# Optimization experiments

Measured on AMD Instinct MI355X. Metric: run time of the kernel, lower is better.

The kernel has to match this reference:

```python
import jax, jax.numpy as jnp
import numpy as np

N, E, P = 50000, 1600000, 500000
IN_DIM, HID, OUT = 512, 128, 64
EPS = 1e-5


def setup_inputs() -> dict:
    key = jax.random.key(0)
    ks = jax.random.split(key, 16)
    d = {}
    d['x'] = jax.random.normal(ks[0], (N, IN_DIM), dtype=jnp.float32)
    d['ei'] = jax.random.randint(ks[1], (2, E), 0, N, dtype=jnp.int32)
    d['src'] = jax.random.randint(ks[2], (P,), 0, N, dtype=jnp.int32)
    d['dst'] = jax.random.randint(ks[3], (P,), 0, N, dtype=jnp.int32)
    # GCNConv layer 1 params
    d['W1'] = jax.random.normal(ks[4], (IN_DIM, HID), dtype=jnp.float32) / np.sqrt(IN_DIM)
    d['b1'] = jnp.zeros((HID,), jnp.float32)
    d['bn1_gamma'] = jnp.ones((HID,), jnp.float32)
    d['bn1_beta'] = jnp.zeros((HID,), jnp.float32)
    d['bn1_mean'] = jnp.zeros((HID,), jnp.float32)
    d['bn1_var'] = jnp.ones((HID,), jnp.float32)
    # GCNConv layer 2 params
    d['W2'] = jax.random.normal(ks[5], (HID, OUT), dtype=jnp.float32) / np.sqrt(HID)
    d['b2'] = jnp.zeros((OUT,), jnp.float32)
    d['bn2_gamma'] = jnp.ones((OUT,), jnp.float32)
    d['bn2_beta'] = jnp.zeros((OUT,), jnp.float32)
    d['bn2_mean'] = jnp.zeros((OUT,), jnp.float32)
    d['bn2_var'] = jnp.ones((OUT,), jnp.float32)
    # edge head MLP
    d['hW1'] = jax.random.normal(ks[6], (2 * OUT, OUT), dtype=jnp.float32) / np.sqrt(2 * OUT)
    d['hb1'] = jnp.zeros((OUT,), jnp.float32)
    d['hW2'] = jax.random.normal(ks[7], (OUT, 1), dtype=jnp.float32) / np.sqrt(OUT)
    d['hb2'] = jnp.zeros((1,), jnp.float32)
    return d


def gcn_conv(x, ei, W, b):
    """PyG-style GCNConv: add self-loops, symmetric deg^-1/2 normalization."""
    xw = x @ W  # [N, F]
    row, col = ei[0], ei[1]
    ones = jnp.ones((ei.shape[1],), x.dtype)
    deg = jax.ops.segment_sum(ones, col, num_segments=N) + 1.0  # +1 for self-loop
    dinv = jax.lax.rsqrt(deg)
    norm = dinv[row] * dinv[col]  # [E]
    agg = jax.ops.segment_sum(norm[:, None] * xw[row], col, num_segments=N)
    # self-loop contribution: dinv[i]^2 * xw[i]
    return agg + (dinv * dinv)[:, None] * xw + b


def bn_eval(x, gamma, beta, mean, var):
    return (x - mean) * jax.lax.rsqrt(var + EPS) * gamma + beta


def reference(x, ei, src, dst, W1, b1, bn1_gamma, bn1_beta, bn1_mean, bn1_var,
              W2, b2, bn2_gamma, bn2_beta, bn2_mean, bn2_var, hW1, hb1, hW2, hb2):
    h = jax.nn.relu(bn_eval(gcn_conv(x, ei, W1, b1), bn1_gamma, bn1_beta, bn1_mean, bn1_var))
    # dropout is identity in eval mode
    z = jax.nn.relu(bn_eval(gcn_conv(h, ei, W2, b2), bn2_gamma, bn2_beta, bn2_mean, bn2_var))
    pair = jnp.concatenate([z[src], z[dst]], axis=1)  # [P, 2*OUT]
    hmid = jax.nn.relu(pair @ hW1 + hb1)
    logits = hmid @ hW2 + hb2  # [P, 1]
    return jax.nn.sigmoid(logits).squeeze(-1)
```

## Files before the change

kernel.cpp:

```cpp
#include <hip/hip_runtime.h>
#include <math.h>


typedef __attribute__((ext_vector_type(8))) short short8x;
typedef __attribute__((ext_vector_type(4))) float f32x4;

__device__ __forceinline__ unsigned short f2bf(float f) {
  unsigned int u = __float_as_uint(f);
  unsigned int r = u + 0x7FFFu + ((u >> 16) & 1u);
  return (unsigned short)(r >> 16);
}
__device__ __forceinline__ float bf2f(unsigned short u) {
  return __uint_as_float(((unsigned int)u) << 16);
}


__global__ void zero_int_kernel(int* __restrict__ p, int n) {
  int i = blockIdx.x * blockDim.x + threadIdx.x;
  if (i < n) p[i] = 0;
}

__global__ __launch_bounds__(256) void binA_hist_kernel(const int* __restrict__ col,
                                                        int* __restrict__ bucket_count, int E,
                                                        int NBK) {
  __shared__ int hist[256];
  const int tid = threadIdx.x;
  hist[tid] = 0;
  __syncthreads();
  const int base = blockIdx.x * 4096;
#pragma unroll
  for (int j = 0; j < 16; ++j) {
    int i = base + j * 256 + tid;
    if (i < E) atomicAdd(&hist[((unsigned int)col[i]) >> 8], 1);
  }
  __syncthreads();
  if (tid < NBK) {
    int h = hist[tid];
    if (h) atomicAdd(&bucket_count[tid], h);
  }
}

__global__ __launch_bounds__(256) void scan_buckets_kernel(const int* __restrict__ bucket_count,
                                                           int* __restrict__ bucket_start,
                                                           int* __restrict__ bcur,
                                                           int* __restrict__ offs_n, int NBK,
                                                           int E) {
  __shared__ int ws[4];
  const int tid = threadIdx.x;
  const int lane = tid & 63;
  const int wid = tid >> 6;
  int v = (tid < NBK) ? bucket_count[tid] : 0;
  int incl = v;
#pragma unroll
  for (int d = 1; d < 64; d <<= 1) {
    int t = __shfl_up(incl, d, 64);
    if (lane >= d) incl += t;
  }
  if (lane == 63) ws[wid] = incl;
  __syncthreads();
  int woff = 0;
#pragma unroll
  for (int w = 0; w < 4; ++w)
    if (w < wid) woff += ws[w];
  int excl = woff + incl - v;
  if (tid < NBK) {
    bucket_start[tid] = excl;
    bcur[tid] = excl;
  }
  if (tid == 0) {
    bucket_start[NBK] = E;
    *offs_n = E;
  }
}

__global__ __launch_bounds__(256) void binA_scatter_kernel(const int* __restrict__ row,
                                                           const int* __restrict__ col,
                                                           int* __restrict__ bcur,
                                                           unsigned int* __restrict__ staging,
                                                           int E, int NBK) {
  __shared__ int hist[256];
  const int tid = threadIdx.x;
  hist[tid] = 0;
  __syncthreads();
  const int base = blockIdx.x * 4096;
  unsigned int payload[16];
  int bk[16];
#pragma unroll
  for (int j = 0; j < 16; ++j) {
    int i = base + j * 256 + tid;
    if (i < E) {
      unsigned int c = (unsigned int)col[i];
      unsigned int r = (unsigned int)row[i];
      payload[j] = (c << 16) | r;
      bk[j] = (int)(c >> 8);
      atomicAdd(&hist[bk[j]], 1);
    } else {
      bk[j] = -1;
    }
  }
  __syncthreads();
  if (tid < NBK) {
    int h = hist[tid];
    hist[tid] = h ? atomicAdd(&bcur[tid], h) : 0;
  }
  __syncthreads();
#pragma unroll
  for (int j = 0; j < 16; ++j) {
    if (bk[j] >= 0) {
      int p = atomicAdd(&hist[bk[j]], 1);
      staging[p] = payload[j];
    }
  }
}

__global__ __launch_bounds__(256) void binB1_kernel(const unsigned int* __restrict__ staging,
                                                    const int* __restrict__ bucket_start,
                                                    int* __restrict__ offs,
                                                    float* __restrict__ dinv, int N) {
  __shared__ int cnt[256];
  __shared__ int ws[4];
  const int b = blockIdx.x;
  const int n0 = b * 256;
  const int tid = threadIdx.x;
  cnt[tid] = 0;
  __syncthreads();
  const int s = bucket_start[b];
  const int e = bucket_start[b + 1];
  for (int t = s + tid; t < e; t += 256) {
    atomicAdd(&cnt[(staging[t] >> 16) & 255u], 1);
  }
  __syncthreads();
  const int deg = cnt[tid];
  const int lane = tid & 63;
  const int wid = tid >> 6;
  int incl = deg;
#pragma unroll
  for (int d = 1; d < 64; d <<= 1) {
    int t = __shfl_up(incl, d, 64);
    if (lane >= d) incl += t;
  }
  if (lane == 63) ws[wid] = incl;
  __syncthreads();
  int woff = 0;
#pragma unroll
  for (int w = 0; w < 4; ++w)
    if (w < wid) woff += ws[w];
  const int excl = woff + incl - deg;
  const int node = n0 + tid;
  if (node < N) {
    offs[node] = s + excl;
    dinv[node] = rsqrtf((float)deg + 1.0f);
  }
}

__global__ __launch_bounds__(512) void binB2_kernel(const unsigned int* __restrict__ staging,
                                                    const int* __restrict__ offs,
                                                    const int* __restrict__ bucket_start,
                                                    const float* __restrict__ dinv,
                                                    unsigned int* __restrict__ csr, int N) {
  __shared__ int cur[256];
  const int b = blockIdx.x;
  const int n0 = b * 256;
  const int tid = threadIdx.x;
  if (tid < 256 && n0 + tid < N) cur[tid] = offs[n0 + tid];
  __syncthreads();
  const int s = bucket_start[b];
  const int e = bucket_start[b + 1];
  for (int t = s + tid; t < e; t += 512) {
    unsigned int v = __builtin_nontemporal_load(&staging[t]);
    int cl = (int)((v >> 16) & 255u);
    unsigned int r = v & 0xFFFFu;
    unsigned int wd = f2bf(dinv[r]);
    int p = atomicAdd(&cur[cl], 1);
    csr[p] = (wd << 16) | r;
  }
}

__global__ void prep_bfrag_kernel(const float* __restrict__ W, unsigned short* __restrict__ out,
                                  int K, int N) {
  int idx = blockIdx.x * blockDim.x + threadIdx.x;
  int KS = K / 32;
  int total = (N / 16) * KS * 64;
  if (idx >= total) return;
  int lane = idx & 63;
  int t = idx >> 6;
  int ks = t % KS;
  int nt = t / KS;
  int n = nt * 16 + (lane & 15);
  int k0 = ks * 32 + (lane >> 4) * 8;
  unsigned short* o = out + (size_t)idx * 8;
#pragma unroll
  for (int j = 0; j < 8; ++j) o[j] = f2bf(W[(size_t)(k0 + j) * N + n]);
}

template <int K, int N, bool ABF16>
__global__ __launch_bounds__(256) void mfma_gemm_kernel(const void* __restrict__ Ap,
                                                        const unsigned short* __restrict__ Bfrag,
                                                        unsigned short* __restrict__ Cout, int M) {
  constexpr int KS = K / 32;
  constexpr int NT = N / 16;
  const int lane = threadIdx.x & 63;
  const int wid = threadIdx.x >> 6;
  const int quad = lane >> 4;
  const int lc = lane & 15;
  const int mbase = blockIdx.x * 128 + wid * 32;
  if (mbase >= M) return;

  f32x4 acc[2][NT];
#pragma unroll
  for (int mt = 0; mt < 2; ++mt)
#pragma unroll
    for (int nt = 0; nt < NT; ++nt) acc[mt][nt] = (f32x4){0.f, 0.f, 0.f, 0.f};

  int r0 = mbase + lc;
  int r1 = mbase + 16 + lc;
  if (r0 >= M) r0 = M - 1;
  if (r1 >= M) r1 = M - 1;

#pragma unroll
  for (int ks = 0; ks < KS; ++ks) {
    const int k0 = ks * 32 + quad * 8;
    short8x a[2];
    if constexpr (ABF16) {
      const unsigned short* A = (const unsigned short*)Ap;
      a[0] = *(const short8x*)(A + (size_t)r0 * K + k0);
      a[1] = *(const short8x*)(A + (size_t)r1 * K + k0);
    } else {
      const float* A = (const float*)Ap;
      const float4* p0 = (const float4*)(A + (size_t)r0 * K + k0);
      const float4* p1 = (const float4*)(A + (size_t)r1 * K + k0);
      float4 u0 = p0[0], v0 = p0[1];
      float4 u1 = p1[0], v1 = p1[1];
      short8x t0, t1;
      t0[0] = (short)f2bf(u0.x); t0[1] = (short)f2bf(u0.y);
      t0[2] = (short)f2bf(u0.z); t0[3] = (short)f2bf(u0.w);
      t0[4] = (short)f2bf(v0.x); t0[5] = (short)f2bf(v0.y);
      t0[6] = (short)f2bf(v0.z); t0[7] = (short)f2bf(v0.w);
      t1[0] = (short)f2bf(u1.x); t1[1] = (short)f2bf(u1.y);
      t1[2] = (short)f2bf(u1.z); t1[3] = (short)f2bf(u1.w);
      t1[4] = (short)f2bf(v1.x); t1[5] = (short)f2bf(v1.y);
      t1[6] = (short)f2bf(v1.z); t1[7] = (short)f2bf(v1.w);
      a[0] = t0;
      a[1] = t1;
    }
#pragma unroll
    for (int nt = 0; nt < NT; ++nt) {
      short8x b = *(const short8x*)(Bfrag + (((size_t)nt * KS + ks) * 64 + lane) * 8);
      acc[0][nt] = __builtin_amdgcn_mfma_f32_16x16x32_bf16(a[0], b, acc[0][nt], 0, 0, 0);
      acc[1][nt] = __builtin_amdgcn_mfma_f32_16x16x32_bf16(a[1], b, acc[1][nt], 0, 0, 0);
    }
  }

#pragma unroll
  for (int mt = 0; mt < 2; ++mt)
#pragma unroll
    for (int nt = 0; nt < NT; ++nt)
#pragma unroll
      for (int reg = 0; reg < 4; ++reg) {
        int row = mbase + mt * 16 + quad * 4 + reg;
        if (row < M) Cout[(size_t)row * N + nt * 16 + lc] = f2bf(acc[mt][nt][reg]);
      }
}

template <int F>
__global__ __launch_bounds__(256) void agg_fast_kernel(
    const unsigned short* __restrict__ xw, const int* __restrict__ offs,
    const unsigned int* __restrict__ csr, const float* __restrict__ dinv,
    const float* __restrict__ bias, const float* __restrict__ gamma,
    const float* __restrict__ beta, const float* __restrict__ mean,
    const float* __restrict__ var, unsigned short* __restrict__ out, int N) {
  constexpr int G = F / 2;
  constexpr int NPB = 256 / G;
  const int li = threadIdx.x % G;
  const int i = blockIdx.x * NPB + threadIdx.x / G;
  if (i >= N) return;
  const unsigned int* xw32 = (const unsigned int*)xw;
  const float di = dinv[i];
  const int s = offs[i], e = offs[i + 1];
  float accL = 0.f, accH = 0.f;
  int t = s;
  for (; t + 16 <= e; t += 16) {
    unsigned int ent[16];
#pragma unroll
    for (int j = 0; j < 16; ++j) ent[j] = csr[t + j];
    unsigned int gv[16];
#pragma unroll
    for (int j = 0; j < 16; ++j) gv[j] = xw32[(size_t)(ent[j] & 0xFFFFu) * G + li];
#pragma unroll
    for (int j = 0; j < 16; ++j) {
      float w = __uint_as_float(ent[j] & 0xFFFF0000u);
      accL += w * __uint_as_float(gv[j] << 16);
      accH += w * __uint_as_float(gv[j] & 0xFFFF0000u);
    }
  }
  for (; t + 4 <= e; t += 4) {
    unsigned int ent[4];
#pragma unroll
    for (int j = 0; j < 4; ++j) ent[j] = csr[t + j];
    unsigned int gv[4];
#pragma unroll
    for (int j = 0; j < 4; ++j) gv[j] = xw32[(size_t)(ent[j] & 0xFFFFu) * G + li];
#pragma unroll
    for (int j = 0; j < 4; ++j) {
      float w = __uint_as_float(ent[j] & 0xFFFF0000u);
      accL += w * __uint_as_float(gv[j] << 16);
      accH += w * __uint_as_float(gv[j] & 0xFFFF0000u);
    }
  }
  for (; t < e; ++t) {
    unsigned int ee = csr[t];
    unsigned int gv = xw32[(size_t)(ee & 0xFFFFu) * G + li];
    float w = __uint_as_float(ee & 0xFFFF0000u);
    accL += w * __uint_as_float(gv << 16);
    accH += w * __uint_as_float(gv & 0xFFFF0000u);
  }
  const int f0 = 2 * li, f1 = f0 + 1;
  unsigned int sv = xw32[(size_t)i * G + li];
  float v0 = di * accL + di * di * __uint_as_float(sv << 16) + bias[f0];
  float v1 = di * accH + di * di * __uint_as_float(sv & 0xFFFF0000u) + bias[f1];
  v0 = (v0 - mean[f0]) * rsqrtf(var[f0] + 1e-5f) * gamma[f0] + beta[f0];
  v1 = (v1 - mean[f1]) * rsqrtf(var[f1] + 1e-5f) * gamma[f1] + beta[f1];
  unsigned int packed =
      (unsigned int)f2bf(fmaxf(v0, 0.f)) | ((unsigned int)f2bf(fmaxf(v1, 0.f)) << 16);
  ((unsigned int*)out)[(size_t)i * G + li] = packed;
}

__global__ __launch_bounds__(256) void head_mfma_kernel(
    const unsigned short* __restrict__ z, const int* __restrict__ src,
    const int* __restrict__ dst, const unsigned short* __restrict__ bfragH,
    const float* __restrict__ hb1, const float* __restrict__ hw2,
    const float* __restrict__ hb2, float* __restrict__ out, int P) {
  const int lane = threadIdx.x & 63;
  const int quad = lane >> 4;
  const int lc = lane & 15;

  short8x bf[4][4];
#pragma unroll
  for (int nt = 0; nt < 4; ++nt)
#pragma unroll
    for (int ks = 0; ks < 4; ++ks)
      bf[nt][ks] = *(const short8x*)(bfragH + (((size_t)nt * 4 + ks) * 64 + lane) * 8);

  float b1v[4], w2v[4];
#pragma unroll
  for (int nt = 0; nt < 4; ++nt) {
    b1v[nt] = hb1[nt * 16 + lc];
    w2v[nt] = hw2[nt * 16 + lc];
  }
  const float bias2 = hb2[0];

  const int nchunks = (P + 15) / 16;
  const int gw = blockIdx.x * 4 + (threadIdx.x >> 6);
  const int nw = gridDim.x * 4;

  for (int ch = gw; ch < nchunks; ch += nw) {
    int p = ch * 16 + lc;
    int pc = p < P ? p : P - 1;
    int s = src[pc], d = dst[pc];
    const unsigned short* zs = z + (size_t)s * 64;
    const unsigned short* zd = z + (size_t)d * 64;
    short8x a[4];
    a[0] = *(const short8x*)(zs + quad * 8);
    a[1] = *(const short8x*)(zs + 32 + quad * 8);
    a[2] = *(const short8x*)(zd + quad * 8);
    a[3] = *(const short8x*)(zd + 32 + quad * 8);

    f32x4 acc[4];
#pragma unroll
    for (int nt = 0; nt < 4; ++nt) acc[nt] = (f32x4){0.f, 0.f, 0.f, 0.f};
#pragma unroll
    for (int nt = 0; nt < 4; ++nt)
#pragma unroll
      for (int t = 0; t < 4; ++t)
        acc[nt] = __builtin_amdgcn_mfma_f32_16x16x32_bf16(a[t], bf[nt][t], acc[nt], 0, 0, 0);

    float part[4];
#pragma unroll
    for (int reg = 0; reg < 4; ++reg) {
      float sum = 0.f;
#pragma unroll
      for (int nt = 0; nt < 4; ++nt) sum += fmaxf(acc[nt][reg] + b1v[nt], 0.f) * w2v[nt];
      part[reg] = sum;
    }
#pragma unroll
    for (int m = 1; m < 16; m <<= 1) {
#pragma unroll
      for (int reg = 0; reg < 4; ++reg) part[reg] += __shfl_xor(part[reg], m, 64);
    }
    if (lc == 0) {
      int pbase = ch * 16 + quad * 4;
      float4 o;
      o.x = 1.0f / (1.0f + __expf(-(part[0] + bias2)));
      o.y = 1.0f / (1.0f + __expf(-(part[1] + bias2)));
      o.z = 1.0f / (1.0f + __expf(-(part[2] + bias2)));
      o.w = 1.0f / (1.0f + __expf(-(part[3] + bias2)));
      if (pbase + 3 < P) {
        *(float4*)(out + pbase) = o;
      } else {
        float ov[4] = {o.x, o.y, o.z, o.w};
        for (int reg = 0; reg < 4; ++reg)
          if (pbase + reg < P) out[pbase + reg] = ov[reg];
      }
    }
  }
}


extern "C" void kernel_launch(void* const* d_in, const int* in_sizes, int n_in,
                              void* d_out, int out_size, void* d_ws, size_t ws_size,
                              hipStream_t stream) {
  const float* x = (const float*)d_in[0];
  const int* ei = (const int*)d_in[1];
  const int* src = (const int*)d_in[2];
  const int* dst = (const int*)d_in[3];
  const float* W1 = (const float*)d_in[4];
  const float* b1 = (const float*)d_in[5];
  const float* g1 = (const float*)d_in[6];
  const float* be1 = (const float*)d_in[7];
  const float* mu1 = (const float*)d_in[8];
  const float* va1 = (const float*)d_in[9];
  const float* W2 = (const float*)d_in[10];
  const float* b2 = (const float*)d_in[11];
  const float* g2 = (const float*)d_in[12];
  const float* be2 = (const float*)d_in[13];
  const float* mu2 = (const float*)d_in[14];
  const float* va2 = (const float*)d_in[15];
  const float* hW1 = (const float*)d_in[16];
  const float* hb1 = (const float*)d_in[17];
  const float* hW2 = (const float*)d_in[18];
  const float* hb2 = (const float*)d_in[19];
  float* out = (float*)d_out;

  const int N = in_sizes[0] / 512;
  const int E = in_sizes[1] / 2;
  const int P = in_sizes[2];
  const int* row = ei;
  const int* col = ei + E;
  const int NBK = (N + 255) / 256;
  const int NAB = (E + 4095) / 4096;

  char* wp = (char*)d_ws;
  auto alloc = [&](size_t bytes) {
    char* p = wp;
    wp += (bytes + 255) & ~(size_t)255;
    return p;
  };
  unsigned short* xw1 = (unsigned short*)alloc((size_t)N * 128 * 2);
  unsigned short* h = (unsigned short*)alloc((size_t)N * 128 * 2);
  unsigned short* xw2 = (unsigned short*)alloc((size_t)N * 64 * 2);
  unsigned short* z = (unsigned short*)alloc((size_t)N * 64 * 2);
  float* dinv = (float*)alloc((size_t)N * 4);
  int* offs = (int*)alloc((size_t)(N + 1) * 4);
  unsigned int* csr = (unsigned int*)alloc((size_t)E * 4);
  unsigned int* staging = (unsigned int*)alloc((size_t)E * 4);
  int* bucket_count = (int*)alloc((size_t)NBK * 4);
  int* bucket_start = (int*)alloc((size_t)(NBK + 1) * 4);
  int* bcur = (int*)alloc((size_t)NBK * 4);
  unsigned short* bfW1 = (unsigned short*)alloc(512 * 128 * 2);
  unsigned short* bfW2 = (unsigned short*)alloc(128 * 64 * 2);
  unsigned short* bfH = (unsigned short*)alloc(128 * 64 * 2);
  (void)ws_size;
  (void)n_in;
  (void)out_size;

  hipLaunchKernelGGL(zero_int_kernel, dim3((NBK + 255) / 256), dim3(256), 0, stream, bucket_count,
                     NBK);
  hipLaunchKernelGGL(binA_hist_kernel, dim3(NAB), dim3(256), 0, stream, col, bucket_count, E, NBK);
  hipLaunchKernelGGL(scan_buckets_kernel, dim3(1), dim3(256), 0, stream, bucket_count,
                     bucket_start, bcur, offs + N, NBK, E);
  hipLaunchKernelGGL(binA_scatter_kernel, dim3(NAB), dim3(256), 0, stream, row, col, bcur, staging,
                     E, NBK);
  hipLaunchKernelGGL(binB1_kernel, dim3(NBK), dim3(256), 0, stream, staging, bucket_start, offs,
                     dinv, N);
  hipLaunchKernelGGL(binB2_kernel, dim3(NBK), dim3(512), 0, stream, staging, offs, bucket_start,
                     dinv, csr, N);

  hipLaunchKernelGGL(prep_bfrag_kernel, dim3((8 * 16 * 64 + 255) / 256), dim3(256), 0, stream, W1,
                     bfW1, 512, 128);
  hipLaunchKernelGGL(prep_bfrag_kernel, dim3((4 * 4 * 64 + 255) / 256), dim3(256), 0, stream, W2,
                     bfW2, 128, 64);
  hipLaunchKernelGGL(prep_bfrag_kernel, dim3((4 * 4 * 64 + 255) / 256), dim3(256), 0, stream, hW1,
                     bfH, 128, 64);

  hipLaunchKernelGGL((mfma_gemm_kernel<512, 128, false>), dim3((N + 127) / 128), dim3(256), 0,
                     stream, x, bfW1, xw1, N);
  hipLaunchKernelGGL((agg_fast_kernel<128>), dim3((N + 3) / 4), dim3(256), 0, stream, xw1, offs,
                     csr, dinv, b1, g1, be1, mu1, va1, h, N);

  hipLaunchKernelGGL((mfma_gemm_kernel<128, 64, true>), dim3((N + 127) / 128), dim3(256), 0, stream,
                     h, bfW2, xw2, N);
  hipLaunchKernelGGL((agg_fast_kernel<64>), dim3((N + 7) / 8), dim3(256), 0, stream, xw2, offs,
                     csr, dinv, b2, g2, be2, mu2, va2, z, N);

  hipLaunchKernelGGL(head_mfma_kernel, dim3(2048), dim3(256), 0, stream, z, src, dst, bfH, hb1,
                     hW2, hb2, out, P);
}
```

Before: 388.2 us.

## Precompute per-node head projections so edge head becomes gather-add

Splits the head's first linear layer into source and destination halves and applies them per node (N rows) with an MFMA GEMM writing fp16, instead of per pair (P rows). The pair head then only gathers two 64-wide halves, adds them with the bias, applies ReLU and dots with hW2. The three weight-prep launches are merged into one, and nontemporal loads are used on the csr, edge and index streams. This cuts head FLOPs and pair work in exchange for an extra N x 128 fp16 buffer and one more GEMM launch, and fp16 storage narrows the representable range of the intermediates.

```diff
diff --git a/kernel.cpp b/kernel.cpp
--- a/kernel.cpp
+++ b/kernel.cpp
@@ -3,6 +3,7 @@
 
 
 typedef __attribute__((ext_vector_type(8))) short short8x;
+typedef __attribute__((ext_vector_type(8))) _Float16 half8x;
 typedef __attribute__((ext_vector_type(4))) float f32x4;
 
 __device__ __forceinline__ unsigned short f2bf(float f) {
@@ -10,8 +11,10 @@
   unsigned int r = u + 0x7FFFu + ((u >> 16) & 1u);
   return (unsigned short)(r >> 16);
 }
-__device__ __forceinline__ float bf2f(unsigned short u) {
-  return __uint_as_float(((unsigned int)u) << 16);
+__device__ __forceinline__ unsigned short f2h(float f) {
+  union { _Float16 h; unsigned short u; } cv;
+  cv.h = (_Float16)f;
+  return cv.u;
 }
 
 
@@ -89,8 +92,8 @@
   for (int j = 0; j < 16; ++j) {
     int i = base + j * 256 + tid;
     if (i < E) {
-      unsigned int c = (unsigned int)col[i];
-      unsigned int r = (unsigned int)row[i];
+      unsigned int c = (unsigned int)__builtin_nontemporal_load(&col[i]);
+      unsigned int r = (unsigned int)__builtin_nontemporal_load(&row[i]);
       payload[j] = (c << 16) | r;
       bk[j] = (int)(c >> 8);
       atomicAdd(&hist[bk[j]], 1);
@@ -176,24 +179,47 @@
   }
 }
 
-__global__ void prep_bfrag_kernel(const float* __restrict__ W, unsigned short* __restrict__ out,
-                                  int K, int N) {
+__global__ __launch_bounds__(256) void prep_all_kernel(const float* __restrict__ W1,
+                                                       const float* __restrict__ W2,
+                                                       const float* __restrict__ hW1,
+                                                       unsigned short* __restrict__ bfW1,
+                                                       unsigned short* __restrict__ bfW2,
+                                                       unsigned short* __restrict__ bfH) {
   int idx = blockIdx.x * blockDim.x + threadIdx.x;
+  const float* W;
+  unsigned short* out;
+  int K, N, base, mode;
+  if (idx < 8192) {
+    W = W1; out = bfW1; K = 512; N = 128; base = 0; mode = 0;
+  } else if (idx < 9216) {
+    W = W2; out = bfW2; K = 128; N = 64; base = 8192; mode = 0;
+  } else if (idx < 10240) {
+    W = hW1; out = bfH; K = 64; N = 128; base = 9216; mode = 1;
+  } else {
+    return;
+  }
+  int id = idx - base;
+  int lane = id & 63;
+  int t = id >> 6;
   int KS = K / 32;
-  int total = (N / 16) * KS * 64;
-  if (idx >= total) return;
-  int lane = idx & 63;
-  int t = idx >> 6;
   int ks = t % KS;
   int nt = t / KS;
   int n = nt * 16 + (lane & 15);
   int k0 = ks * 32 + (lane >> 4) * 8;
-  unsigned short* o = out + (size_t)idx * 8;
-#pragma unroll
-  for (int j = 0; j < 8; ++j) o[j] = f2bf(W[(size_t)(k0 + j) * N + n]);
-}
-
-template <int K, int N, bool ABF16>
+  unsigned short* o = out + (size_t)id * 8;
+#pragma unroll
+  for (int j = 0; j < 8; ++j) {
+    int k = k0 + j;
+    float v;
+    if (mode == 0)
+      v = W[(size_t)k * N + n];
+    else
+      v = (n < 64) ? W[(size_t)k * 64 + n] : W[(size_t)(64 + k) * 64 + (n - 64)];
+    o[j] = f2bf(v);
+  }
+}
+
+template <int K, int N, bool ABF16, bool OUTF16>
 __global__ __launch_bounds__(256) void mfma_gemm_kernel(const void* __restrict__ Ap,
                                                         const unsigned short* __restrict__ Bfrag,
                                                         unsigned short* __restrict__ Cout, int M) {
@@ -258,7 +284,10 @@
 #pragma unroll
       for (int reg = 0; reg < 4; ++reg) {
         int row = mbase + mt * 16 + quad * 4 + reg;
-        if (row < M) Cout[(size_t)row * N + nt * 16 + lc] = f2bf(acc[mt][nt][reg]);
+        if (row < M) {
+          float v = acc[mt][nt][reg];
+          Cout[(size_t)row * N + nt * 16 + lc] = OUTF16 ? f2h(v) : f2bf(v);
+        }
       }
 }
 
@@ -282,7 +311,7 @@
   for (; t + 16 <= e; t += 16) {
     unsigned int ent[16];
 #pragma unroll
-    for (int j = 0; j < 16; ++j) ent[j] = csr[t + j];
+    for (int j = 0; j < 16; ++j) ent[j] = __builtin_nontemporal_load(&csr[t + j]);
     unsigned int gv[16];
 #pragma unroll
     for (int j = 0; j < 16; ++j) gv[j] = xw32[(size_t)(ent[j] & 0xFFFFu) * G + li];
@@ -296,7 +325,7 @@
   for (; t + 4 <= e; t += 4) {
     unsigned int ent[4];
 #pragma unroll
-    for (int j = 0; j < 4; ++j) ent[j] = csr[t + j];
+    for (int j = 0; j < 4; ++j) ent[j] = __builtin_nontemporal_load(&csr[t + j]);
     unsigned int gv[4];
 #pragma unroll
     for (int j = 0; j < 4; ++j) gv[j] = xw32[(size_t)(ent[j] & 0xFFFFu) * G + li];
@@ -308,7 +337,7 @@
     }
   }
   for (; t < e; ++t) {
-    unsigned int ee = csr[t];
+    unsigned int ee = __builtin_nontemporal_load(&csr[t]);
     unsigned int gv = xw32[(size_t)(ee & 0xFFFFu) * G + li];
     float w = __uint_as_float(ee & 0xFFFF0000u);
     accL += w * __uint_as_float(gv << 16);
@@ -325,30 +354,21 @@
   ((unsigned int*)out)[(size_t)i * G + li] = packed;
 }
 
-__global__ __launch_bounds__(256) void head_mfma_kernel(
-    const unsigned short* __restrict__ z, const int* __restrict__ src,
-    const int* __restrict__ dst, const unsigned short* __restrict__ bfragH,
-    const float* __restrict__ hb1, const float* __restrict__ hw2,
-    const float* __restrict__ hb2, float* __restrict__ out, int P) {
+__global__ __launch_bounds__(256) void head2_kernel(
+    const unsigned short* __restrict__ zh, const int* __restrict__ src,
+    const int* __restrict__ dst, const float* __restrict__ hb1,
+    const float* __restrict__ hw2, const float* __restrict__ hb2,
+    float* __restrict__ out, int P) {
   const int lane = threadIdx.x & 63;
+  const int lc = lane & 15;
   const int quad = lane >> 4;
-  const int lc = lane & 15;
-
-  short8x bf[4][4];
-#pragma unroll
-  for (int nt = 0; nt < 4; ++nt)
-#pragma unroll
-    for (int ks = 0; ks < 4; ++ks)
-      bf[nt][ks] = *(const short8x*)(bfragH + (((size_t)nt * 4 + ks) * 64 + lane) * 8);
-
-  float b1v[4], w2v[4];
-#pragma unroll
-  for (int nt = 0; nt < 4; ++nt) {
-    b1v[nt] = hb1[nt * 16 + lc];
-    w2v[nt] = hw2[nt * 16 + lc];
+  float b1v[16], w2v[16];
+#pragma unroll
+  for (int t = 0; t < 16; ++t) {
+    b1v[t] = hb1[quad * 16 + t];
+    w2v[t] = hw2[quad * 16 + t];
   }
   const float bias2 = hb2[0];
-
   const int nchunks = (P + 15) / 16;
   const int gw = blockIdx.x * 4 + (threadIdx.x >> 6);
   const int nw = gridDim.x * 4;
@@ -356,51 +376,28 @@
   for (int ch = gw; ch < nchunks; ch += nw) {
     int p = ch * 16 + lc;
     int pc = p < P ? p : P - 1;
-    int s = src[pc], d = dst[pc];
-    const unsigned short* zs = z + (size_t)s * 64;
-    const unsigned short* zd = z + (size_t)d * 64;
-    short8x a[4];
-    a[0] = *(const short8x*)(zs + quad * 8);
-    a[1] = *(const short8x*)(zs + 32 + quad * 8);
-    a[2] = *(const short8x*)(zd + quad * 8);
-    a[3] = *(const short8x*)(zd + 32 + quad * 8);
-
-    f32x4 acc[4];
-#pragma unroll
-    for (int nt = 0; nt < 4; ++nt) acc[nt] = (f32x4){0.f, 0.f, 0.f, 0.f};
-#pragma unroll
-    for (int nt = 0; nt < 4; ++nt)
-#pragma unroll
-      for (int t = 0; t < 4; ++t)
-        acc[nt] = __builtin_amdgcn_mfma_f32_16x16x32_bf16(a[t], bf[nt][t], acc[nt], 0, 0, 0);
-
-    float part[4];
-#pragma unroll
-    for (int reg = 0; reg < 4; ++reg) {
-      float sum = 0.f;
-#pragma unroll
-      for (int nt = 0; nt < 4; ++nt) sum += fmaxf(acc[nt][reg] + b1v[nt], 0.f) * w2v[nt];
-      part[reg] = sum;
-    }
-#pragma unroll
-    for (int m = 1; m < 16; m <<= 1) {
-#pragma unroll
-      for (int reg = 0; reg < 4; ++reg) part[reg] += __shfl_xor(part[reg], m, 64);
-    }
-    if (lc == 0) {
-      int pbase = ch * 16 + quad * 4;
-      float4 o;
-      o.x = 1.0f / (1.0f + __expf(-(part[0] + bias2)));
-      o.y = 1.0f / (1.0f + __expf(-(part[1] + bias2)));
-      o.z = 1.0f / (1.0f + __expf(-(part[2] + bias2)));
-      o.w = 1.0f / (1.0f + __expf(-(part[3] + bias2)));
-      if (pbase + 3 < P) {
-        *(float4*)(out + pbase) = o;
-      } else {
-        float ov[4] = {o.x, o.y, o.z, o.w};
-        for (int reg = 0; reg < 4; ++reg)
-          if (pbase + reg < P) out[pbase + reg] = ov[reg];
-      }
+    int s = __builtin_nontemporal_load(&src[pc]);
+    int d = __builtin_nontemporal_load(&dst[pc]);
+    const half8x* pa = (const half8x*)(zh + (size_t)s * 128 + quad * 16);
+    const half8x* pb = (const half8x*)(zh + (size_t)d * 128 + 64 + quad * 16);
+    half8x a0 = pa[0], a1 = pa[1];
+    half8x b0 = pb[0], b1 = pb[1];
+    float acc = 0.f;
+#pragma unroll
+    for (int t = 0; t < 8; ++t) {
+      float hm = fmaxf((float)a0[t] + (float)b0[t] + b1v[t], 0.f);
+      acc = fmaf(hm, w2v[t], acc);
+    }
+#pragma unroll
+    for (int t = 0; t < 8; ++t) {
+      float hm = fmaxf((float)a1[t] + (float)b1[t] + b1v[8 + t], 0.f);
+      acc = fmaf(hm, w2v[8 + t], acc);
+    }
+    acc += __shfl_xor(acc, 16, 64);
+    acc += __shfl_xor(acc, 32, 64);
+    if (quad == 0 && p < P) {
+      float o = 1.0f / (1.0f + __expf(-(acc + bias2)));
+      __builtin_nontemporal_store(o, &out[p]);
     }
   }
 }
@@ -449,6 +446,7 @@
   unsigned short* h = (unsigned short*)alloc((size_t)N * 128 * 2);
   unsigned short* xw2 = (unsigned short*)alloc((size_t)N * 64 * 2);
   unsigned short* z = (unsigned short*)alloc((size_t)N * 64 * 2);
+  unsigned short* zh = (unsigned short*)alloc((size_t)N * 128 * 2);
   float* dinv = (float*)alloc((size_t)N * 4);
   int* offs = (int*)alloc((size_t)(N + 1) * 4);
   unsigned int* csr = (unsigned int*)alloc((size_t)E * 4);
@@ -475,23 +473,21 @@
   hipLaunchKernelGGL(binB2_kernel, dim3(NBK), dim3(512), 0, stream, staging, offs, bucket_start,
                      dinv, csr, N);
 
-  hipLaunchKernelGGL(prep_bfrag_kernel, dim3((8 * 16 * 64 + 255) / 256), dim3(256), 0, stream, W1,
-                     bfW1, 512, 128);
-  hipLaunchKernelGGL(prep_bfrag_kernel, dim3((4 * 4 * 64 + 255) / 256), dim3(256), 0, stream, W2,
-                     bfW2, 128, 64);
-  hipLaunchKernelGGL(prep_bfrag_kernel, dim3((4 * 4 * 64 + 255) / 256), dim3(256), 0, stream, hW1,
-                     bfH, 128, 64);
-
-  hipLaunchKernelGGL((mfma_gemm_kernel<512, 128, false>), dim3((N + 127) / 128), dim3(256), 0,
-                     stream, x, bfW1, xw1, N);
+  hipLaunchKernelGGL(prep_all_kernel, dim3(40), dim3(256), 0, stream, W1, W2, hW1, bfW1, bfW2,
+                     bfH);
+
+  hipLaunchKernelGGL((mfma_gemm_kernel<512, 128, false, false>), dim3((N + 127) / 128), dim3(256),
+                     0, stream, x, bfW1, xw1, N);
   hipLaunchKernelGGL((agg_fast_kernel<128>), dim3((N + 3) / 4), dim3(256), 0, stream, xw1, offs,
                      csr, dinv, b1, g1, be1, mu1, va1, h, N);
 
-  hipLaunchKernelGGL((mfma_gemm_kernel<128, 64, true>), dim3((N + 127) / 128), dim3(256), 0, stream,
-                     h, bfW2, xw2, N);
+  hipLaunchKernelGGL((mfma_gemm_kernel<128, 64, true, false>), dim3((N + 127) / 128), dim3(256), 0,
+                     stream, h, bfW2, xw2, N);
   hipLaunchKernelGGL((agg_fast_kernel<64>), dim3((N + 7) / 8), dim3(256), 0, stream, xw2, offs,
                      csr, dinv, b2, g2, be2, mu2, va2, z, N);
 
-  hipLaunchKernelGGL(head_mfma_kernel, dim3(2048), dim3(256), 0, stream, z, src, dst, bfH, hb1,
-                     hW2, hb2, out, P);
-}
+  hipLaunchKernelGGL((mfma_gemm_kernel<64, 128, true, true>), dim3((N + 127) / 128), dim3(256), 0,
+                     stream, z, bfH, zh, N);
+  hipLaunchKernelGGL(head2_kernel, dim3(2048), dim3(256), 0, stream, zh, src, dst, hb1, hW2, hb2,
+                     out, P);
+}
```

Result: slower. 402.8 us (+3.8%).
